# Kernel tuning notes

Measured on AMD Instinct MI355X. Metric: run time of the kernel, lower is better.

## Reference

```python
import jax, jax.numpy as jnp
import numpy as np

B, T, C = 4, 2048, 1024
H = 16
D = C // H  # head_dim = 64


def setup_inputs() -> dict:
    key = jax.random.key(0)
    ks = jax.random.split(key, 9)
    s = 1.0 / np.sqrt(C)
    return {
        "x": jax.random.normal(ks[0], (B, T, C), dtype=jnp.float32),
        "Wq": jax.random.normal(ks[1], (C, C), dtype=jnp.float32) * s,
        "bq": jnp.zeros((C,), dtype=jnp.float32),
        "Wk": jax.random.normal(ks[2], (C, C), dtype=jnp.float32) * s,
        "bk": jnp.zeros((C,), dtype=jnp.float32),
        "Wv": jax.random.normal(ks[3], (C, C), dtype=jnp.float32) * s,
        "bv": jnp.zeros((C,), dtype=jnp.float32),
        "Wp": jax.random.normal(ks[4], (C, C), dtype=jnp.float32) * s,
        "bp": jnp.zeros((C,), dtype=jnp.float32),
    }


def reference(x, Wq, bq, Wk, bk, Wv, bv, Wp, bp):
    # Linear projections; reshape to [B, H, T, D]
    def split_heads(y):
        return y.reshape(B, T, H, D).transpose(0, 2, 1, 3)

    q = split_heads(x @ Wq + bq)
    k = split_heads(x @ Wk + bk)
    v = split_heads(x @ Wv + bv)

    scale = 1.0 / np.sqrt(D)
    att = jnp.einsum('bhqd,bhkd->bhqk', q, k) * scale  # [B,H,T,T]
    att = jax.nn.softmax(att, axis=-1)
    # dropout with p=0.0 is identity
    out = jnp.einsum('bhqk,bhkd->bhqd', att, v)        # [B,H,T,D]
    out = out.transpose(0, 2, 1, 3).reshape(B, T, C)
    return out @ Wp + bp
```

## Files before the change

### kernel.cpp

```cpp
#include <hip/hip_runtime.h>


#define B_ 4
#define T_ 2048
#define C_ 1024
#define H_ 16
#define D_ 64

typedef float  f32x4  __attribute__((ext_vector_type(4)));
typedef __bf16 bf16x8 __attribute__((ext_vector_type(8)));
typedef __bf16 bf16x4 __attribute__((ext_vector_type(4)));

typedef const __attribute__((address_space(1))) void gv_t;
typedef __attribute__((address_space(3))) void lds_t;

__device__ __forceinline__ void async_load16(const void* g, void* l) {
  __builtin_amdgcn_global_load_lds((gv_t*)g, (lds_t*)l, 16, 0, 0);
}

__device__ __forceinline__ float fast_exp2(float x) {
#if __has_builtin(__builtin_amdgcn_exp2f)
  return __builtin_amdgcn_exp2f(x);
#else
  return exp2f(x);
#endif
}

__global__ __launch_bounds__(256) void cast_f32_bf16(
    const float* __restrict__ in, __bf16* __restrict__ out, int n) {
  int i = (blockIdx.x * 256 + threadIdx.x) * 8;
  if (i >= n) return;
  float4 a = *(const float4*)(in + i);
  float4 b = *(const float4*)(in + i + 4);
  bf16x8 o;
  o[0] = (__bf16)a.x; o[1] = (__bf16)a.y; o[2] = (__bf16)a.z; o[3] = (__bf16)a.w;
  o[4] = (__bf16)b.x; o[5] = (__bf16)b.y; o[6] = (__bf16)b.z; o[7] = (__bf16)b.w;
  *(bf16x8*)(out + i) = o;
}

__global__ __launch_bounds__(256) void transpose_cast_w(
    const float* __restrict__ W0, const float* __restrict__ W1,
    const float* __restrict__ W2, const float* __restrict__ W3,
    __bf16* __restrict__ out) {
  int z = blockIdx.z;
  const float* W = (z == 0) ? W0 : (z == 1) ? W1 : (z == 2) ? W2 : W3;
  __bf16* o = out + (size_t)z * (C_ * C_);
  __shared__ __align__(16) __bf16 sT[64][72];
  int tid = threadIdx.x;
  int n0 = blockIdx.x * 64, k0 = blockIdx.y * 64;
#pragma unroll
  for (int i = 0; i < 4; i++) {
    int s = tid + i * 256;
    int kr = s >> 4, nc = (s & 15) * 4;
    float4 v = *(const float4*)&W[(size_t)(k0 + kr) * C_ + n0 + nc];
    bf16x4 t;
    t[0] = (__bf16)v.x; t[1] = (__bf16)v.y; t[2] = (__bf16)v.z; t[3] = (__bf16)v.w;
    *(bf16x4*)&sT[kr][nc] = t;
  }
  __syncthreads();
#pragma unroll
  for (int i = 0; i < 2; i++) {
    int s = tid + i * 256;
    int nr = s >> 3, kc = (s & 7) * 8;
    bf16x8 ov;
#pragma unroll
    for (int j = 0; j < 8; j++) ov[j] = sT[kc + j][nr];
    *(bf16x8*)&o[(size_t)(n0 + nr) * C_ + k0 + kc] = ov;
  }
}

__global__ __launch_bounds__(256) void transpose_v(
    const __bf16* __restrict__ V, __bf16* __restrict__ Vt) {
  int bh = blockIdx.y;
  int b = bh >> 4, h = bh & 15;
  int t0 = blockIdx.x * 64;
  __shared__ __align__(16) __bf16 sT[64][72];
  int tid = threadIdx.x;
#pragma unroll
  for (int i = 0; i < 2; i++) {
    int s = tid + i * 256;
    int tt = s >> 3, d8 = (s & 7) * 8;
    *(bf16x8*)&sT[tt][d8] =
        *(const bf16x8*)&V[(size_t)(b * T_ + t0 + tt) * C_ + h * D_ + d8];
  }
  __syncthreads();
#pragma unroll
  for (int i = 0; i < 2; i++) {
    int s = tid + i * 256;
    int dr = s >> 3, t8 = (s & 7) * 8;
    bf16x8 ov;
#pragma unroll
    for (int j = 0; j < 8; j++) ov[j] = sT[t8 + j][dr];
    *(bf16x8*)&Vt[((size_t)bh * D_ + dr) * T_ + t0 + t8] = ov;
  }
}

template <typename OutT>
__device__ __forceinline__ void gemm_body(
    const __bf16* __restrict__ A, const __bf16* __restrict__ Bt,
    const float* __restrict__ bias, OutT* __restrict__ C, int M, int N, int K) {
  __shared__ __align__(16) __bf16 sA[128 * 32];
  __shared__ __align__(16) __bf16 sB[128 * 32];
  int tid = threadIdx.x, lane = tid & 63, wave = tid >> 6;
  int lr = lane & 15, quad = lane >> 4;
  int m0 = blockIdx.y * 128, n0 = blockIdx.x * 128;
  int wm = (wave & 1) * 64, wn = (wave >> 1) * 64;

  const f32x4 zero = {0.f, 0.f, 0.f, 0.f};
  f32x4 acc[4][4];
#pragma unroll
  for (int i = 0; i < 4; i++)
#pragma unroll
    for (int j = 0; j < 4; j++) acc[i][j] = zero;

  for (int k0 = 0; k0 < K; k0 += 32) {
    __syncthreads();
#pragma unroll
    for (int i = 0; i < 2; i++) {
      int s = tid + i * 256;
      int r = s >> 2, c8 = (s & 3) * 8;
      async_load16(A + (size_t)(m0 + r) * K + k0 + c8, &sA[s * 8]);
      async_load16(Bt + (size_t)(n0 + r) * K + k0 + c8, &sB[s * 8]);
    }
    __syncthreads();
    bf16x8 af[4], bfr[4];
#pragma unroll
    for (int mt = 0; mt < 4; mt++)
      af[mt] = *(const bf16x8*)&sA[(wm + mt * 16 + lr) * 32 + quad * 8];
#pragma unroll
    for (int nt = 0; nt < 4; nt++)
      bfr[nt] = *(const bf16x8*)&sB[(wn + nt * 16 + lr) * 32 + quad * 8];
#pragma unroll
    for (int mt = 0; mt < 4; mt++)
#pragma unroll
      for (int nt = 0; nt < 4; nt++)
        acc[mt][nt] = __builtin_amdgcn_mfma_f32_16x16x32_bf16(
            af[mt], bfr[nt], acc[mt][nt], 0, 0, 0);
  }
#pragma unroll
  for (int mt = 0; mt < 4; mt++) {
#pragma unroll
    for (int nt = 0; nt < 4; nt++) {
      int n = n0 + wn + nt * 16 + lr;
      float bv = bias[n];
#pragma unroll
      for (int r = 0; r < 4; r++) {
        int m = m0 + wm + mt * 16 + quad * 4 + r;
        C[(size_t)m * N + n] = (OutT)(acc[mt][nt][r] + bv);
      }
    }
  }
}

__global__ __launch_bounds__(256) void gemm_qkv_kernel(
    const __bf16* __restrict__ A, const __bf16* __restrict__ WT,
    const float* __restrict__ b0, const float* __restrict__ b1,
    const float* __restrict__ b2, __bf16* __restrict__ outbase) {
  int z = blockIdx.z;
  const float* bias = (z == 0) ? b0 : (z == 1) ? b1 : b2;
  gemm_body<__bf16>(A, WT + (size_t)z * C_ * C_, bias,
                    outbase + (size_t)z * (B_ * T_) * C_, B_ * T_, C_, C_);
}

__global__ __launch_bounds__(256) void gemm_proj_kernel(
    const __bf16* __restrict__ A, const __bf16* __restrict__ Bt,
    const float* __restrict__ bias, float* __restrict__ C) {
  gemm_body<float>(A, Bt, bias, C, B_ * T_, C_, C_);
}

__global__ __launch_bounds__(256) void attn_kernel(
    const __bf16* __restrict__ Q, const __bf16* __restrict__ K,
    const __bf16* __restrict__ Vt, __bf16* __restrict__ O) {
  __shared__ __align__(16) __bf16 sK[64 * 72];
  __shared__ __align__(16) __bf16 sV[64 * 72];
  __shared__ __align__(16) __bf16 sP[4][16 * 72];
  int tid = threadIdx.x, wave = tid >> 6, lane = tid & 63;
  int lr = lane & 15, quad = lane >> 4;
  int bh = blockIdx.y;
  int b = bh >> 4, h = bh & 15;
  int qw = blockIdx.x * 64 + wave * 16;
  __bf16* sPw = &sP[wave][0];

  bf16x8 aq0, aq1;
  {
    const __bf16* qp = Q + ((size_t)(b * T_ + qw + lr)) * C_ + h * D_ + quad * 8;
    aq0 = *(const bf16x8*)qp;
    aq1 = *(const bf16x8*)(qp + 32);
  }

  bf16x8 onesf;
#pragma unroll
  for (int j = 0; j < 8; j++) onesf[j] = (__bf16)1.0f;

  const f32x4 zero = {0.f, 0.f, 0.f, 0.f};
  f32x4 accO[4];
  f32x4 accL = zero;
#pragma unroll
  for (int d = 0; d < 4; d++) accO[d] = zero;

  const float cexp = 0.125f * 1.44269504088896340736f;

  int srow[2], sc8[2];
#pragma unroll
  for (int i = 0; i < 2; i++) {
    int s = tid + i * 256;
    srow[i] = s >> 3;
    sc8[i] = (s & 7) * 8;
  }

  bf16x8 kreg[2], vreg[2];
#pragma unroll
  for (int i = 0; i < 2; i++) {
    kreg[i] = *(const bf16x8*)(K + ((size_t)(b * T_ + srow[i])) * C_ + h * D_ + sc8[i]);
    vreg[i] = *(const bf16x8*)(Vt + ((size_t)(bh * D_ + srow[i])) * T_ + sc8[i]);
  }

  for (int k0 = 0; k0 < T_; k0 += 64) {
    __syncthreads();
#pragma unroll
    for (int i = 0; i < 2; i++) {
      *(bf16x8*)&sK[srow[i] * 72 + sc8[i]] = kreg[i];
      *(bf16x8*)&sV[srow[i] * 72 + sc8[i]] = vreg[i];
    }
    __syncthreads();

    if (k0 + 64 < T_) {
      int kn = k0 + 64;
#pragma unroll
      for (int i = 0; i < 2; i++) {
        kreg[i] = *(const bf16x8*)(K + ((size_t)(b * T_ + kn + srow[i])) * C_ + h * D_ + sc8[i]);
        vreg[i] = *(const bf16x8*)(Vt + ((size_t)(bh * D_ + srow[i])) * T_ + kn + sc8[i]);
      }
    }

    f32x4 accS[4];
#pragma unroll
    for (int nt = 0; nt < 4; nt++) {
      bf16x8 bk0 = *(const bf16x8*)&sK[(nt * 16 + lr) * 72 + quad * 8];
      bf16x8 bk1 = *(const bf16x8*)&sK[(nt * 16 + lr) * 72 + 32 + quad * 8];
      f32x4 z = zero;
      z = __builtin_amdgcn_mfma_f32_16x16x32_bf16(aq0, bk0, z, 0, 0, 0);
      z = __builtin_amdgcn_mfma_f32_16x16x32_bf16(aq1, bk1, z, 0, 0, 0);
      accS[nt] = z;
    }

#pragma unroll
    for (int nt = 0; nt < 4; nt++)
#pragma unroll
      for (int r = 0; r < 4; r++)
        sPw[(quad * 4 + r) * 72 + nt * 16 + lr] =
            (__bf16)fast_exp2(accS[nt][r] * cexp);

    bf16x8 ap0 = *(const bf16x8*)&sPw[lr * 72 + quad * 8];
    bf16x8 ap1 = *(const bf16x8*)&sPw[lr * 72 + 32 + quad * 8];
    accL = __builtin_amdgcn_mfma_f32_16x16x32_bf16(ap0, onesf, accL, 0, 0, 0);
    accL = __builtin_amdgcn_mfma_f32_16x16x32_bf16(ap1, onesf, accL, 0, 0, 0);
#pragma unroll
    for (int dt = 0; dt < 4; dt++) {
      bf16x8 bv0 = *(const bf16x8*)&sV[(dt * 16 + lr) * 72 + quad * 8];
      bf16x8 bv1 = *(const bf16x8*)&sV[(dt * 16 + lr) * 72 + 32 + quad * 8];
      accO[dt] = __builtin_amdgcn_mfma_f32_16x16x32_bf16(ap0, bv0, accO[dt], 0, 0, 0);
      accO[dt] = __builtin_amdgcn_mfma_f32_16x16x32_bf16(ap1, bv1, accO[dt], 0, 0, 0);
    }
  }

#pragma unroll
  for (int r = 0; r < 4; r++) {
    float inv = 1.0f / accL[r];
#pragma unroll
    for (int dt = 0; dt < 4; dt++) {
      O[((size_t)(b * T_ + qw + quad * 4 + r)) * C_ + h * D_ + dt * 16 + lr] =
          (__bf16)(accO[dt][r] * inv);
    }
  }
}

extern "C" void kernel_launch(void* const* d_in, const int* in_sizes, int n_in,
                              void* d_out, int out_size, void* d_ws, size_t ws_size,
                              hipStream_t stream) {
  const float* x  = (const float*)d_in[0];
  const float* Wq = (const float*)d_in[1];
  const float* bq = (const float*)d_in[2];
  const float* Wk = (const float*)d_in[3];
  const float* bk = (const float*)d_in[4];
  const float* Wv = (const float*)d_in[5];
  const float* bv = (const float*)d_in[6];
  const float* Wp = (const float*)d_in[7];
  const float* bp = (const float*)d_in[8];
  float* out = (float*)d_out;

  char* ws = (char*)d_ws;
  const size_t MB = 1024 * 1024;
  __bf16* xb    = (__bf16*)(ws + 0 * MB);
  __bf16* WT    = (__bf16*)(ws + 16 * MB);
  __bf16* Qb    = (__bf16*)(ws + 24 * MB);
  __bf16* Kb    = Qb + (size_t)(B_ * T_) * C_;
  __bf16* Vb    = Kb + (size_t)(B_ * T_) * C_;
  __bf16* Vt    = xb;
  __bf16* attnb = (__bf16*)(ws + 72 * MB);
  __bf16* WpT   = WT + (size_t)3 * C_ * C_;

  cast_f32_bf16<<<dim3(4096), dim3(256), 0, stream>>>(x, xb, B_ * T_ * C_);
  transpose_cast_w<<<dim3(16, 16, 4), dim3(256), 0, stream>>>(Wq, Wk, Wv, Wp, WT);
  gemm_qkv_kernel<<<dim3(8, 64, 3), dim3(256), 0, stream>>>(xb, WT, bq, bk, bv, Qb);
  transpose_v<<<dim3(32, 64), dim3(256), 0, stream>>>(Vb, Vt);
  attn_kernel<<<dim3(32, 64), dim3(256), 0, stream>>>(Qb, Kb, Vt, attnb);
  gemm_proj_kernel<<<dim3(8, 64), dim3(256), 0, stream>>>(attnb, WpT, bp, out);
}
```

Baseline: 329.9 us.

## Fuse V transpose into QKV GEMM epilogue and transpose attention MFMA operands

The V projection GEMM now writes its output directly in transposed [B, C, T] layout from its epilogue, which removes the separate transpose_v kernel and one round trip of V through global memory. The attention kernel swaps MFMA operand order so S and O are computed transposed. This lets the exp'd P tile be stored with packed bf16x4 writes and the output be written as bf16x4 vectors, replacing scalar stores. The risk is that the transposed V stores in the GEMM epilogue are strided across T and may coalesce poorly.

```diff
diff --git a/kernel.cpp b/kernel.cpp
--- a/kernel.cpp
+++ b/kernel.cpp
@@ -69,33 +69,7 @@
   }
 }
 
-__global__ __launch_bounds__(256) void transpose_v(
-    const __bf16* __restrict__ V, __bf16* __restrict__ Vt) {
-  int bh = blockIdx.y;
-  int b = bh >> 4, h = bh & 15;
-  int t0 = blockIdx.x * 64;
-  __shared__ __align__(16) __bf16 sT[64][72];
-  int tid = threadIdx.x;
-#pragma unroll
-  for (int i = 0; i < 2; i++) {
-    int s = tid + i * 256;
-    int tt = s >> 3, d8 = (s & 7) * 8;
-    *(bf16x8*)&sT[tt][d8] =
-        *(const bf16x8*)&V[(size_t)(b * T_ + t0 + tt) * C_ + h * D_ + d8];
-  }
-  __syncthreads();
-#pragma unroll
-  for (int i = 0; i < 2; i++) {
-    int s = tid + i * 256;
-    int dr = s >> 3, t8 = (s & 7) * 8;
-    bf16x8 ov;
-#pragma unroll
-    for (int j = 0; j < 8; j++) ov[j] = sT[t8 + j][dr];
-    *(bf16x8*)&Vt[((size_t)bh * D_ + dr) * T_ + t0 + t8] = ov;
-  }
-}
-
-template <typename OutT>
+template <typename OutT, int EPI>
 __device__ __forceinline__ void gemm_body(
     const __bf16* __restrict__ A, const __bf16* __restrict__ Bt,
     const float* __restrict__ bias, OutT* __restrict__ C, int M, int N, int K) {
@@ -137,16 +111,34 @@
         acc[mt][nt] = __builtin_amdgcn_mfma_f32_16x16x32_bf16(
             af[mt], bfr[nt], acc[mt][nt], 0, 0, 0);
   }
-#pragma unroll
-  for (int mt = 0; mt < 4; mt++) {
-#pragma unroll
-    for (int nt = 0; nt < 4; nt++) {
-      int n = n0 + wn + nt * 16 + lr;
-      float bv = bias[n];
-#pragma unroll
-      for (int r = 0; r < 4; r++) {
-        int m = m0 + wm + mt * 16 + quad * 4 + r;
-        C[(size_t)m * N + n] = (OutT)(acc[mt][nt][r] + bv);
+  if (EPI == 0) {
+#pragma unroll
+    for (int mt = 0; mt < 4; mt++) {
+#pragma unroll
+      for (int nt = 0; nt < 4; nt++) {
+        int n = n0 + wn + nt * 16 + lr;
+        float bv = bias[n];
+#pragma unroll
+        for (int r = 0; r < 4; r++) {
+          int m = m0 + wm + mt * 16 + quad * 4 + r;
+          C[(size_t)m * N + n] = (OutT)(acc[mt][nt][r] + bv);
+        }
+      }
+    }
+  } else {
+    int bb = m0 >> 11;
+    int mloc0 = (m0 & (T_ - 1)) + wm;
+    __bf16* Ct = (__bf16*)C;
+#pragma unroll
+    for (int mt = 0; mt < 4; mt++) {
+#pragma unroll
+      for (int nt = 0; nt < 4; nt++) {
+        int n = n0 + wn + nt * 16 + lr;
+        float bv = bias[n];
+        bf16x4 ov;
+#pragma unroll
+        for (int r = 0; r < 4; r++) ov[r] = (__bf16)(acc[mt][nt][r] + bv);
+        *(bf16x4*)&Ct[((size_t)bb * C_ + n) * T_ + mloc0 + mt * 16 + quad * 4] = ov;
       }
     }
   }
@@ -155,17 +147,22 @@
 __global__ __launch_bounds__(256) void gemm_qkv_kernel(
     const __bf16* __restrict__ A, const __bf16* __restrict__ WT,
     const float* __restrict__ b0, const float* __restrict__ b1,
-    const float* __restrict__ b2, __bf16* __restrict__ outbase) {
+    const float* __restrict__ b2, __bf16* __restrict__ qkbase,
+    __bf16* __restrict__ Vt) {
   int z = blockIdx.z;
-  const float* bias = (z == 0) ? b0 : (z == 1) ? b1 : b2;
-  gemm_body<__bf16>(A, WT + (size_t)z * C_ * C_, bias,
-                    outbase + (size_t)z * (B_ * T_) * C_, B_ * T_, C_, C_);
+  if (z == 2) {
+    gemm_body<__bf16, 1>(A, WT + (size_t)2 * C_ * C_, b2, Vt, B_ * T_, C_, C_);
+  } else {
+    const float* bias = (z == 0) ? b0 : b1;
+    gemm_body<__bf16, 0>(A, WT + (size_t)z * C_ * C_, bias,
+                         qkbase + (size_t)z * (B_ * T_) * C_, B_ * T_, C_, C_);
+  }
 }
 
 __global__ __launch_bounds__(256) void gemm_proj_kernel(
     const __bf16* __restrict__ A, const __bf16* __restrict__ Bt,
     const float* __restrict__ bias, float* __restrict__ C) {
-  gemm_body<float>(A, Bt, bias, C, B_ * T_, C_, C_);
+  gemm_body<float, 0>(A, Bt, bias, C, B_ * T_, C_, C_);
 }
 
 __global__ __launch_bounds__(256) void attn_kernel(
@@ -239,39 +236,40 @@
       bf16x8 bk0 = *(const bf16x8*)&sK[(nt * 16 + lr) * 72 + quad * 8];
       bf16x8 bk1 = *(const bf16x8*)&sK[(nt * 16 + lr) * 72 + 32 + quad * 8];
       f32x4 z = zero;
-      z = __builtin_amdgcn_mfma_f32_16x16x32_bf16(aq0, bk0, z, 0, 0, 0);
-      z = __builtin_amdgcn_mfma_f32_16x16x32_bf16(aq1, bk1, z, 0, 0, 0);
+      z = __builtin_amdgcn_mfma_f32_16x16x32_bf16(bk0, aq0, z, 0, 0, 0);
+      z = __builtin_amdgcn_mfma_f32_16x16x32_bf16(bk1, aq1, z, 0, 0, 0);
       accS[nt] = z;
     }
 
 #pragma unroll
-    for (int nt = 0; nt < 4; nt++)
-#pragma unroll
-      for (int r = 0; r < 4; r++)
-        sPw[(quad * 4 + r) * 72 + nt * 16 + lr] =
-            (__bf16)fast_exp2(accS[nt][r] * cexp);
-
-    bf16x8 ap0 = *(const bf16x8*)&sPw[lr * 72 + quad * 8];
-    bf16x8 ap1 = *(const bf16x8*)&sPw[lr * 72 + 32 + quad * 8];
-    accL = __builtin_amdgcn_mfma_f32_16x16x32_bf16(ap0, onesf, accL, 0, 0, 0);
-    accL = __builtin_amdgcn_mfma_f32_16x16x32_bf16(ap1, onesf, accL, 0, 0, 0);
+    for (int nt = 0; nt < 4; nt++) {
+      bf16x4 pk;
+#pragma unroll
+      for (int r = 0; r < 4; r++) pk[r] = (__bf16)fast_exp2(accS[nt][r] * cexp);
+      *(bf16x4*)&sPw[lr * 72 + nt * 16 + quad * 4] = pk;
+    }
+
+    bf16x8 bp0 = *(const bf16x8*)&sPw[lr * 72 + quad * 8];
+    bf16x8 bp1 = *(const bf16x8*)&sPw[lr * 72 + 32 + quad * 8];
+    accL = __builtin_amdgcn_mfma_f32_16x16x32_bf16(onesf, bp0, accL, 0, 0, 0);
+    accL = __builtin_amdgcn_mfma_f32_16x16x32_bf16(onesf, bp1, accL, 0, 0, 0);
 #pragma unroll
     for (int dt = 0; dt < 4; dt++) {
-      bf16x8 bv0 = *(const bf16x8*)&sV[(dt * 16 + lr) * 72 + quad * 8];
-      bf16x8 bv1 = *(const bf16x8*)&sV[(dt * 16 + lr) * 72 + 32 + quad * 8];
-      accO[dt] = __builtin_amdgcn_mfma_f32_16x16x32_bf16(ap0, bv0, accO[dt], 0, 0, 0);
-      accO[dt] = __builtin_amdgcn_mfma_f32_16x16x32_bf16(ap1, bv1, accO[dt], 0, 0, 0);
-    }
-  }
-
-#pragma unroll
-  for (int r = 0; r < 4; r++) {
-    float inv = 1.0f / accL[r];
-#pragma unroll
-    for (int dt = 0; dt < 4; dt++) {
-      O[((size_t)(b * T_ + qw + quad * 4 + r)) * C_ + h * D_ + dt * 16 + lr] =
-          (__bf16)(accO[dt][r] * inv);
-    }
+      bf16x8 av0 = *(const bf16x8*)&sV[(dt * 16 + lr) * 72 + quad * 8];
+      bf16x8 av1 = *(const bf16x8*)&sV[(dt * 16 + lr) * 72 + 32 + quad * 8];
+      accO[dt] = __builtin_amdgcn_mfma_f32_16x16x32_bf16(av0, bp0, accO[dt], 0, 0, 0);
+      accO[dt] = __builtin_amdgcn_mfma_f32_16x16x32_bf16(av1, bp1, accO[dt], 0, 0, 0);
+    }
+  }
+
+  float inv = 1.0f / accL[0];
+  __bf16* op = O + ((size_t)(b * T_ + qw + lr)) * C_ + h * D_ + quad * 4;
+#pragma unroll
+  for (int dt = 0; dt < 4; dt++) {
+    bf16x4 ov;
+#pragma unroll
+    for (int r = 0; r < 4; r++) ov[r] = (__bf16)(accO[dt][r] * inv);
+    *(bf16x4*)&op[dt * 16] = ov;
   }
 }
 
@@ -295,15 +293,13 @@
   __bf16* WT    = (__bf16*)(ws + 16 * MB);
   __bf16* Qb    = (__bf16*)(ws + 24 * MB);
   __bf16* Kb    = Qb + (size_t)(B_ * T_) * C_;
-  __bf16* Vb    = Kb + (size_t)(B_ * T_) * C_;
-  __bf16* Vt    = xb;
+  __bf16* Vt    = Kb + (size_t)(B_ * T_) * C_;
   __bf16* attnb = (__bf16*)(ws + 72 * MB);
   __bf16* WpT   = WT + (size_t)3 * C_ * C_;
 
   cast_f32_bf16<<<dim3(4096), dim3(256), 0, stream>>>(x, xb, B_ * T_ * C_);
   transpose_cast_w<<<dim3(16, 16, 4), dim3(256), 0, stream>>>(Wq, Wk, Wv, Wp, WT);
-  gemm_qkv_kernel<<<dim3(8, 64, 3), dim3(256), 0, stream>>>(xb, WT, bq, bk, bv, Qb);
-  transpose_v<<<dim3(32, 64), dim3(256), 0, stream>>>(Vb, Vt);
+  gemm_qkv_kernel<<<dim3(8, 64, 3), dim3(256), 0, stream>>>(xb, WT, bq, bk, bv, Qb, Vt);
   attn_kernel<<<dim3(32, 64), dim3(256), 0, stream>>>(Qb, Kb, Vt, attnb);
   gemm_proj_kernel<<<dim3(8, 64), dim3(256), 0, stream>>>(attnb, WpT, bp, out);
 }
```

Result: no change. 325.4 us (-1.4%).
